# Kernel tuning notes

Measured on AMD Instinct MI355X. Metric: run time of the kernel, lower is better.

## Reference

```python
import jax, jax.numpy as jnp
import numpy as np

N, E, NFEAT, HID, HEADS, NCLASS = 100000, 1600000, 256, 64, 1, 32


def gat_conv(x, src, dst, W, a_src, a_dst, b, H, C, concat):
    n = x.shape[0]
    h = (x @ W).reshape(n, H, C)                      # [N,H,C]
    a_s = (h * a_src).sum(-1)                          # [N,H]
    a_d = (h * a_dst).sum(-1)                          # [N,H]
    e = jax.nn.leaky_relu(a_s[src] + a_d[dst], 0.2)    # [E,H]
    emax = jax.ops.segment_max(e, dst, num_segments=n)
    emax = jnp.where(jnp.isfinite(emax), emax, 0.0)
    ex = jnp.exp(e - emax[dst])
    denom = jax.ops.segment_sum(ex, dst, num_segments=n)
    alpha = ex / (denom[dst] + 1e-16)                  # segment softmax over in-edges of dst
    msg = h[src] * alpha[:, :, None]                   # [E,H,C]
    out = jax.ops.segment_sum(msg, dst, num_segments=n)
    out = out.reshape(n, H * C) if concat else out.mean(axis=1)
    return out + b


def setup_inputs() -> dict:
    key = jax.random.key(0)
    ks = jax.random.split(key, 14)
    x = jax.random.normal(ks[0], (N, NFEAT), dtype=jnp.float32)
    edge_index = jax.random.randint(ks[1], (2, E), 0, N, dtype=jnp.int64)
    s = 0.05
    return {
        'x': x, 'edge_index': edge_index,
        'W1': jax.random.normal(ks[2], (NFEAT, HEADS * HID), jnp.float32) * s,
        'as1': jax.random.normal(ks[3], (HEADS, HID), jnp.float32) * s,
        'ad1': jax.random.normal(ks[4], (HEADS, HID), jnp.float32) * s,
        'b1': jnp.zeros((HEADS * HID,), jnp.float32),
        'W2': jax.random.normal(ks[5], (HEADS * HID, HEADS * HID), jnp.float32) * s,
        'as2': jax.random.normal(ks[6], (HEADS, HID), jnp.float32) * s,
        'ad2': jax.random.normal(ks[7], (HEADS, HID), jnp.float32) * s,
        'b2': jnp.zeros((HEADS * HID,), jnp.float32),
        'W3': jax.random.normal(ks[8], (HEADS * HID, HEADS * NCLASS), jnp.float32) * s,
        'as3': jax.random.normal(ks[9], (HEADS, NCLASS), jnp.float32) * s,
        'ad3': jax.random.normal(ks[10], (HEADS, NCLASS), jnp.float32) * s,
        'b3': jnp.zeros((NCLASS,), jnp.float32),
    }


def reference(x, edge_index, W1, as1, ad1, b1, W2, as2, ad2, b2, W3, as3, ad3, b3):
    # add self loops (PyG GATConv add_self_loops=True)
    loop = jnp.arange(N, dtype=edge_index.dtype)
    src = jnp.concatenate([edge_index[0], loop])
    dst = jnp.concatenate([edge_index[1], loop])
    out = jax.nn.leaky_relu(gat_conv(x, src, dst, W1, as1, ad1, b1, HEADS, HID, True), 0.01)
    out = jax.nn.leaky_relu(gat_conv(out, src, dst, W2, as2, ad2, b2, HEADS, HID, True), 0.01)
    out = gat_conv(out, src, dst, W3, as3, ad3, b3, HEADS, NCLASS, False)
    return out
```

## Files before the change

kernel.cpp:

```cpp
#include <hip/hip_runtime.h>

#define NN 100000
#define NE 1600000
#define NF 256
#define HD 64
#define NC 32

#define BKS 8
#define NBK ((NN + 255) >> 8)
#define CHUNK 4096
#define NBLK ((NE + CHUNK - 1) / CHUNK)

__device__ __forceinline__ float lrelu02(float x) { return fmaxf(x, 0.2f * x); }


__global__ __launch_bounds__(256) void bucket_hist(const int* __restrict__ dst, int* __restrict__ gcnt) {
    __shared__ int hist[NBK];
    int tid = threadIdx.x;
    for (int i = tid; i < NBK; i += 256) hist[i] = 0;
    __syncthreads();
    int base = blockIdx.x * CHUNK;
    #pragma unroll
    for (int k = 0; k < CHUNK / 256; k++) {
        int i = base + k * 256 + tid;
        if (i < NE) atomicAdd(&hist[dst[i] >> BKS], 1);
    }
    __syncthreads();
    for (int i = tid; i < NBK; i += 256) if (hist[i]) atomicAdd(&gcnt[i], hist[i]);
}

__global__ void bucket_scan(const int* __restrict__ gcnt, int* __restrict__ gbase, int* __restrict__ gcur) {
    __shared__ int sh[512];
    int tid = threadIdx.x;
    int v = (tid < NBK) ? gcnt[tid] : 0;
    sh[tid] = v;
    __syncthreads();
    for (int d = 1; d < 512; d <<= 1) {
        int t = (tid >= d) ? sh[tid - d] : 0;
        __syncthreads();
        sh[tid] += t;
        __syncthreads();
    }
    if (tid < NBK) { int ex = sh[tid] - v; gbase[tid] = ex; gcur[tid] = ex; }
}

__global__ __launch_bounds__(256) void bin_edges(const int* __restrict__ src, const int* __restrict__ dst,
                                                 int* __restrict__ gcur, int2* __restrict__ ebuf) {
    __shared__ int hist[NBK];
    __shared__ int excl[NBK];
    __shared__ int runbase[NBK];
    __shared__ int ssum[256];
    __shared__ int2 sorted[CHUNK];
    int tid = threadIdx.x;
    int base = blockIdx.x * CHUNK;
    int n = NE - base; if (n > CHUNK) n = CHUNK;

    for (int i = tid; i < NBK; i += 256) hist[i] = 0;
    __syncthreads();

    int2 ed[CHUNK / 256];
    int bk[CHUNK / 256];
    #pragma unroll
    for (int k = 0; k < CHUNK / 256; k++) {
        int i = base + k * 256 + tid;
        if (i < NE) {
            ed[k] = make_int2(src[i], dst[i]);
            bk[k] = ed[k].y >> BKS;
            atomicAdd(&hist[bk[k]], 1);
        } else bk[k] = -1;
    }
    __syncthreads();
    int h0 = (2 * tid < NBK) ? hist[2 * tid] : 0;
    int h1 = (2 * tid + 1 < NBK) ? hist[2 * tid + 1] : 0;
    ssum[tid] = h0 + h1;
    __syncthreads();
    for (int d = 1; d < 256; d <<= 1) {
        int t = (tid >= d) ? ssum[tid - d] : 0;
        __syncthreads();
        ssum[tid] += t;
        __syncthreads();
    }
    int pref = ssum[tid] - (h0 + h1);
    if (2 * tid < NBK) excl[2 * tid] = pref;
    if (2 * tid + 1 < NBK) excl[2 * tid + 1] = pref + h0;
    for (int b = tid; b < NBK; b += 256) {
        int c = hist[b];
        runbase[b] = c ? atomicAdd(&gcur[b], c) : 0;
    }
    __syncthreads();
    #pragma unroll
    for (int k = 0; k < CHUNK / 256; k++) {
        if (bk[k] >= 0) {
            int r = atomicAdd(&excl[bk[k]], 1);
            sorted[r] = ed[k];
        }
    }
    __syncthreads();
    for (int i = tid; i < n; i += 256) {
        int2 e = sorted[i];
        int b = e.y >> BKS;
        int local_rank = i - (excl[b] - hist[b]);
        ebuf[runbase[b] + local_rank] = e;
    }
}

__global__ __launch_bounds__(256) void bucket_csr(const int2* __restrict__ ebuf, const int* __restrict__ gbase,
                                                  const int* __restrict__ gcnt,
                                                  int* __restrict__ offs, int* __restrict__ csr) {
    __shared__ int hist[256], cur[256], ssum[256];
    int b = blockIdx.x, tid = threadIdx.x;
    int ebeg = gbase[b], cnt = gcnt[b];
    int node0 = b << BKS;
    hist[tid] = 0;
    __syncthreads();
    for (int i = ebeg + tid; i < ebeg + cnt; i += 256)
        atomicAdd(&hist[ebuf[i].y & 255], 1);
    __syncthreads();
    int v = hist[tid];
    ssum[tid] = v;
    __syncthreads();
    for (int d = 1; d < 256; d <<= 1) {
        int t = (tid >= d) ? ssum[tid - d] : 0;
        __syncthreads();
        ssum[tid] += t;
        __syncthreads();
    }
    int ex = ebeg + ssum[tid] - v;
    cur[tid] = ex;
    int nnode = NN - node0; if (nnode > 256) nnode = 256;
    if (tid < nnode) offs[node0 + tid] = ex;
    if (b == NBK - 1 && tid == nnode - 1) offs[NN] = ebeg + cnt;
    __syncthreads();
    for (int i = ebeg + tid; i < ebeg + cnt; i += 256) {
        int2 e = ebuf[i];
        int pos = atomicAdd(&cur[e.y & 255], 1);
        csr[pos] = e.x;
    }
}


template <int CIN, int COUT, int NPT, int CPT>
__global__ __launch_bounds__(256) void rb_gemm3(const float* __restrict__ in, const float* __restrict__ W,
                                                const float* __restrict__ a_s, const float* __restrict__ a_d,
                                                float* __restrict__ h, float* __restrict__ asv,
                                                float* __restrict__ adv) {
    const int KC  = 32;
    const int CG  = COUT / CPT;
    const int NG  = 256 / CG;
    const int BN  = NG * NPT;
    const int BNP = BN + 4;
    const int NP4 = NPT / 4;
    const int CP4 = CPT / 4;
    __shared__ float xsT[KC * BNP];
    __shared__ float Wl[KC * COUT];

    int tid = threadIdx.x;
    int cg  = tid % CG;
    int ng  = tid / CG;
    int c0  = cg * CPT;
    int n0  = ng * NPT;
    int n0base = blockIdx.x * BN;

    float4 acc[NPT][CP4];
    #pragma unroll
    for (int i = 0; i < NPT; i++)
        #pragma unroll
        for (int j = 0; j < CP4; j++) acc[i][j] = make_float4(0.f, 0.f, 0.f, 0.f);

    for (int k0 = 0; k0 < CIN; k0 += KC) {
        __syncthreads();
        #pragma unroll
        for (int f = tid; f < BN * KC / 4; f += 256) {
            int n = f >> 3;
            int q = f & 7;
            int gn = n0base + n;
            float4 v = make_float4(0.f, 0.f, 0.f, 0.f);
            if (gn < NN) v = *(const float4*)&in[(size_t)gn * CIN + k0 + q * 4];
            xsT[(q * 4 + 0) * BNP + n] = v.x;
            xsT[(q * 4 + 1) * BNP + n] = v.y;
            xsT[(q * 4 + 2) * BNP + n] = v.z;
            xsT[(q * 4 + 3) * BNP + n] = v.w;
        }
        #pragma unroll
        for (int f = tid; f < KC * COUT / 4; f += 256)
            *(float4*)&Wl[f * 4] = *(const float4*)&W[(size_t)k0 * COUT + f * 4];
        __syncthreads();
        #pragma unroll 2
        for (int k = 0; k < KC; k++) {
            float4 xv[NP4];
            #pragma unroll
            for (int p = 0; p < NP4; p++) xv[p] = *(const float4*)&xsT[k * BNP + n0 + p * 4];
            float4 wv[CP4];
            #pragma unroll
            for (int j = 0; j < CP4; j++) wv[j] = *(const float4*)&Wl[k * COUT + c0 + j * 4];
            #pragma unroll
            for (int i = 0; i < NPT; i++) {
                float xc = (i & 3) == 0 ? xv[i >> 2].x : (i & 3) == 1 ? xv[i >> 2].y
                         : (i & 3) == 2 ? xv[i >> 2].z : xv[i >> 2].w;
                #pragma unroll
                for (int j = 0; j < CP4; j++) {
                    acc[i][j].x += xc * wv[j].x; acc[i][j].y += xc * wv[j].y;
                    acc[i][j].z += xc * wv[j].z; acc[i][j].w += xc * wv[j].w;
                }
            }
        }
    }

    float4 As[CP4], Ad[CP4];
    #pragma unroll
    for (int j = 0; j < CP4; j++) {
        As[j] = *(const float4*)&a_s[c0 + j * 4];
        Ad[j] = *(const float4*)&a_d[c0 + j * 4];
    }
    #pragma unroll
    for (int i = 0; i < NPT; i++) {
        int gn = n0base + n0 + i;
        if (gn < NN) {
            #pragma unroll
            for (int j = 0; j < CP4; j++)
                *(float4*)&h[(size_t)gn * COUT + c0 + j * 4] = acc[i][j];
        }
        float vs = 0.f, vd = 0.f;
        #pragma unroll
        for (int j = 0; j < CP4; j++) {
            vs += acc[i][j].x * As[j].x + acc[i][j].y * As[j].y
                + acc[i][j].z * As[j].z + acc[i][j].w * As[j].w;
            vd += acc[i][j].x * Ad[j].x + acc[i][j].y * Ad[j].y
                + acc[i][j].z * Ad[j].z + acc[i][j].w * Ad[j].w;
        }
        #pragma unroll
        for (int off = 1; off < CG; off <<= 1) { vs += __shfl_xor(vs, off); vd += __shfl_xor(vd, off); }
        if (cg == 0 && gn < NN) { asv[gn] = vs; adv[gn] = vd; }
    }
}


template <int C, bool ACT>
__global__ __launch_bounds__(256) void gat_agg(const float* __restrict__ h, const float* __restrict__ asv,
                                               const float* __restrict__ adv, const int* __restrict__ offs,
                                               const int* __restrict__ csr,
                                               const float* __restrict__ bias, float* __restrict__ out) {
    const int LPR = C / 4;
    const int G = 64 / LPR;
    const float4* h4 = (const float4*)h;
    int lane = threadIdx.x & 63;
    int v = blockIdx.x * 4 + (threadIdx.x >> 6);
    int beg = offs[v], end = offs[v + 1];
    int g = lane / LPR, r = lane % LPR;
    float adv_v = adv[v];

    float4 acc = {0.f, 0.f, 0.f, 0.f};
    float dsum = 0.f;
    #pragma unroll 4
    for (int e = beg + g; e < end; e += G) {
        int s = csr[e];
        float ww = __expf(lrelu02(asv[s] + adv_v));
        float4 hv = h4[(size_t)s * LPR + r];
        dsum += ww;
        acc.x += ww * hv.x; acc.y += ww * hv.y; acc.z += ww * hv.z; acc.w += ww * hv.w;
    }
    #pragma unroll
    for (int off = LPR; off < 64; off <<= 1) {
        acc.x += __shfl_xor(acc.x, off);
        acc.y += __shfl_xor(acc.y, off);
        acc.z += __shfl_xor(acc.z, off);
        acc.w += __shfl_xor(acc.w, off);
        dsum += __shfl_xor(dsum, off);
    }
    if (g == 0) {
        float selfw = __expf(lrelu02(asv[v] + adv_v));
        float4 hs = h4[(size_t)v * LPR + r];
        acc.x += selfw * hs.x; acc.y += selfw * hs.y;
        acc.z += selfw * hs.z; acc.w += selfw * hs.w;
        dsum += selfw;
        float inv = 1.f / (dsum + 1e-16f);
        float4 bb = ((const float4*)bias)[r];
        float4 o;
        o.x = acc.x * inv + bb.x; o.y = acc.y * inv + bb.y;
        o.z = acc.z * inv + bb.z; o.w = acc.w * inv + bb.w;
        if (ACT) {
            o.x = fmaxf(o.x, 0.01f * o.x); o.y = fmaxf(o.y, 0.01f * o.y);
            o.z = fmaxf(o.z, 0.01f * o.z); o.w = fmaxf(o.w, 0.01f * o.w);
        }
        ((float4*)out)[(size_t)v * LPR + r] = o;
    }
}


extern "C" void kernel_launch(void* const* d_in, const int* in_sizes, int n_in,
                              void* d_out, int out_size, void* d_ws, size_t ws_size,
                              hipStream_t stream) {
    const float* x   = (const float*)d_in[0];
    const int*   ei  = (const int*)d_in[1];
    const float* W1  = (const float*)d_in[2];
    const float* as1 = (const float*)d_in[3];
    const float* ad1 = (const float*)d_in[4];
    const float* b1  = (const float*)d_in[5];
    const float* W2  = (const float*)d_in[6];
    const float* as2 = (const float*)d_in[7];
    const float* ad2 = (const float*)d_in[8];
    const float* b2  = (const float*)d_in[9];
    const float* W3  = (const float*)d_in[10];
    const float* as3 = (const float*)d_in[11];
    const float* ad3 = (const float*)d_in[12];
    const float* b3  = (const float*)d_in[13];
    float* out = (float*)d_out;

    const int* srcp = ei;
    const int* dstp = ei + NE;

    char* w = (char*)d_ws;
    float* h     = (float*)w;   w += sizeof(float) * (size_t)NN * HD;
    float* featB = (float*)w;   w += sizeof(float) * (size_t)NN * HD;
    float* asv   = (float*)w;   w += sizeof(float) * NN;
    float* advv  = (float*)w;   w += sizeof(float) * NN;
    int* offs    = (int*)w;     w += sizeof(int) * (NN + 1);
    int* csr     = (int*)w;     w += sizeof(int) * (size_t)NE;
    int2* ebuf   = (int2*)w;    w += sizeof(int2) * (size_t)NE;
    int* gcnt    = (int*)w;     w += sizeof(int) * NBK;
    int* gbase   = (int*)w;     w += sizeof(int) * NBK;
    int* gcur    = (int*)w;     w += sizeof(int) * NBK;

    const int GB = (NN + 255) / 256;

    hipMemsetAsync(gcnt, 0, sizeof(int) * NBK, stream);
    bucket_hist<<<NBLK, 256, 0, stream>>>(dstp, gcnt);
    bucket_scan<<<1, 512, 0, stream>>>(gcnt, gbase, gcur);
    bin_edges<<<NBLK, 256, 0, stream>>>(srcp, dstp, gcur, ebuf);
    bucket_csr<<<NBK, 256, 0, stream>>>(ebuf, gbase, gcnt, offs, csr);

    rb_gemm3<NF, HD, 8, 8><<<GB, 256, 0, stream>>>(x, W1, as1, ad1, h, asv, advv);
    gat_agg<HD, true><<<NN / 4, 256, 0, stream>>>(h, asv, advv, offs, csr, b1, featB);

    rb_gemm3<HD, HD, 8, 8><<<GB, 256, 0, stream>>>(featB, W2, as2, ad2, h, asv, advv);
    gat_agg<HD, true><<<NN / 4, 256, 0, stream>>>(h, asv, advv, offs, csr, b2, featB);

    rb_gemm3<HD, NC, 4, 8><<<GB, 256, 0, stream>>>(featB, W3, as3, ad3, h, asv, advv);
    gat_agg<NC, false><<<NN / 4, 256, 0, stream>>>(h, asv, advv, offs, csr, b3, out);
}
```

Before: 500.4 us.

## Replace FP32 register-blocked GEMMs with split-bf16 MFMA GEMMs

Replaces the scalar FP32 register-tiled projection GEMM with a matrix-core kernel using bf16 MFMA 16x16x32. Accuracy is kept near FP32 by splitting each operand into high and low bf16 parts and issuing three MFMAs per tile. The attention-score dot products stay fused into the epilogue. The intent is to move the GEMM FLOPs onto matrix cores. In exchange, every tile load now pays for conversion and splitting, and the output stores become scalar, strided writes per lane.

Result: faster. 461.2 us (-7.8%).

```diff
diff --git a/kernel.cpp b/kernel.cpp
--- a/kernel.cpp
+++ b/kernel.cpp
@@ -12,6 +12,18 @@
 #define NBLK ((NE + CHUNK - 1) / CHUNK)
 
 __device__ __forceinline__ float lrelu02(float x) { return fmaxf(x, 0.2f * x); }
+
+typedef __attribute__((ext_vector_type(8))) short bf16x8;
+typedef __attribute__((ext_vector_type(4))) float f32x4;
+
+__device__ __forceinline__ unsigned short f2bf(float f) {
+    unsigned int u = __float_as_uint(f);
+    unsigned int r = u + 0x7FFFu + ((u >> 16) & 1u);
+    return (unsigned short)(r >> 16);
+}
+__device__ __forceinline__ float bf2f(unsigned short s) {
+    return __uint_as_float(((unsigned int)s) << 16);
+}
 
 
 __global__ __launch_bounds__(256) void bucket_hist(const int* __restrict__ dst, int* __restrict__ gcnt) {
@@ -139,98 +151,119 @@
 }
 
 
-template <int CIN, int COUT, int NPT, int CPT>
-__global__ __launch_bounds__(256) void rb_gemm3(const float* __restrict__ in, const float* __restrict__ W,
-                                                const float* __restrict__ a_s, const float* __restrict__ a_d,
-                                                float* __restrict__ h, float* __restrict__ asv,
-                                                float* __restrict__ adv) {
+template <int CIN, int COUT>
+__global__ __launch_bounds__(256) void mfma_gemm(const float* __restrict__ in, const float* __restrict__ W,
+                                                 const float* __restrict__ a_s, const float* __restrict__ a_d,
+                                                 float* __restrict__ h, float* __restrict__ asv,
+                                                 float* __restrict__ adv) {
     const int KC  = 32;
-    const int CG  = COUT / CPT;
-    const int NG  = 256 / CG;
-    const int BN  = NG * NPT;
-    const int BNP = BN + 4;
-    const int NP4 = NPT / 4;
-    const int CP4 = CPT / 4;
-    __shared__ float xsT[KC * BNP];
-    __shared__ float Wl[KC * COUT];
+    const int BM  = 128;
+    const int RS  = 40;
+    const int NCT = COUT / 16;
+    const int NCH = CIN / KC;
+    __shared__ unsigned short Ah[BM * RS];
+    __shared__ unsigned short Al[BM * RS];
+    __shared__ unsigned short Bh[COUT * RS];
+    __shared__ unsigned short Bl[COUT * RS];
 
     int tid = threadIdx.x;
-    int cg  = tid % CG;
-    int ng  = tid / CG;
-    int c0  = cg * CPT;
-    int n0  = ng * NPT;
-    int n0base = blockIdx.x * BN;
-
-    float4 acc[NPT][CP4];
-    #pragma unroll
-    for (int i = 0; i < NPT; i++)
-        #pragma unroll
-        for (int j = 0; j < CP4; j++) acc[i][j] = make_float4(0.f, 0.f, 0.f, 0.f);
-
-    for (int k0 = 0; k0 < CIN; k0 += KC) {
-        __syncthreads();
-        #pragma unroll
-        for (int f = tid; f < BN * KC / 4; f += 256) {
-            int n = f >> 3;
+    int lane = tid & 63;
+    int wave = tid >> 6;
+    int fr = lane & 15;
+    int kg = lane >> 4;
+    int n0base = blockIdx.x * BM;
+
+    f32x4 acc[2][NCT];
+    #pragma unroll
+    for (int rt = 0; rt < 2; rt++)
+        #pragma unroll
+        for (int ct = 0; ct < NCT; ct++) acc[rt][ct] = (f32x4){0.f, 0.f, 0.f, 0.f};
+
+    for (int t = 0; t < NCH; t++) {
+        int k0 = t * KC;
+        __syncthreads();
+        unsigned int* Ahu = (unsigned int*)Ah;
+        unsigned int* Alu = (unsigned int*)Al;
+        #pragma unroll
+        for (int f = tid; f < BM * KC / 4; f += 256) {
+            int row = f >> 3;
             int q = f & 7;
-            int gn = n0base + n;
+            int gn = n0base + row;
             float4 v = make_float4(0.f, 0.f, 0.f, 0.f);
             if (gn < NN) v = *(const float4*)&in[(size_t)gn * CIN + k0 + q * 4];
-            xsT[(q * 4 + 0) * BNP + n] = v.x;
-            xsT[(q * 4 + 1) * BNP + n] = v.y;
-            xsT[(q * 4 + 2) * BNP + n] = v.z;
-            xsT[(q * 4 + 3) * BNP + n] = v.w;
-        }
-        #pragma unroll
-        for (int f = tid; f < KC * COUT / 4; f += 256)
-            *(float4*)&Wl[f * 4] = *(const float4*)&W[(size_t)k0 * COUT + f * 4];
-        __syncthreads();
-        #pragma unroll 2
-        for (int k = 0; k < KC; k++) {
-            float4 xv[NP4];
+            unsigned short h0 = f2bf(v.x), h1 = f2bf(v.y), h2 = f2bf(v.z), h3 = f2bf(v.w);
+            unsigned short l0 = f2bf(v.x - bf2f(h0)), l1 = f2bf(v.y - bf2f(h1));
+            unsigned short l2 = f2bf(v.z - bf2f(h2)), l3 = f2bf(v.w - bf2f(h3));
+            int wi = row * (RS / 2) + q * 2;
+            Ahu[wi]     = (unsigned int)h0 | ((unsigned int)h1 << 16);
+            Ahu[wi + 1] = (unsigned int)h2 | ((unsigned int)h3 << 16);
+            Alu[wi]     = (unsigned int)l0 | ((unsigned int)l1 << 16);
+            Alu[wi + 1] = (unsigned int)l2 | ((unsigned int)l3 << 16);
+        }
+        #pragma unroll
+        for (int f = tid; f < KC * COUT / 4; f += 256) {
+            int k = f / (COUT / 4);
+            int c = (f % (COUT / 4)) * 4;
+            float4 v = *(const float4*)&W[(size_t)(k0 + k) * COUT + c];
+            unsigned short h0 = f2bf(v.x), h1 = f2bf(v.y), h2 = f2bf(v.z), h3 = f2bf(v.w);
+            Bh[(c + 0) * RS + k] = h0;  Bl[(c + 0) * RS + k] = f2bf(v.x - bf2f(h0));
+            Bh[(c + 1) * RS + k] = h1;  Bl[(c + 1) * RS + k] = f2bf(v.y - bf2f(h1));
+            Bh[(c + 2) * RS + k] = h2;  Bl[(c + 2) * RS + k] = f2bf(v.z - bf2f(h2));
+            Bh[(c + 3) * RS + k] = h3;  Bl[(c + 3) * RS + k] = f2bf(v.w - bf2f(h3));
+        }
+        __syncthreads();
+        bf16x8 ah[2], al[2], bh[NCT], bl[NCT];
+        #pragma unroll
+        for (int rt = 0; rt < 2; rt++) {
+            int row = wave * 32 + rt * 16 + fr;
+            ah[rt] = *(const bf16x8*)&Ah[row * RS + kg * 8];
+            al[rt] = *(const bf16x8*)&Al[row * RS + kg * 8];
+        }
+        #pragma unroll
+        for (int ct = 0; ct < NCT; ct++) {
+            int col = ct * 16 + fr;
+            bh[ct] = *(const bf16x8*)&Bh[col * RS + kg * 8];
+            bl[ct] = *(const bf16x8*)&Bl[col * RS + kg * 8];
+        }
+        #pragma unroll
+        for (int rt = 0; rt < 2; rt++)
             #pragma unroll
-            for (int p = 0; p < NP4; p++) xv[p] = *(const float4*)&xsT[k * BNP + n0 + p * 4];
-            float4 wv[CP4];
+            for (int ct = 0; ct < NCT; ct++) {
+                acc[rt][ct] = __builtin_amdgcn_mfma_f32_16x16x32_bf16(ah[rt], bh[ct], acc[rt][ct], 0, 0, 0);
+                acc[rt][ct] = __builtin_amdgcn_mfma_f32_16x16x32_bf16(ah[rt], bl[ct], acc[rt][ct], 0, 0, 0);
+                acc[rt][ct] = __builtin_amdgcn_mfma_f32_16x16x32_bf16(al[rt], bh[ct], acc[rt][ct], 0, 0, 0);
+            }
+    }
+
+    float As_l[NCT], Ad_l[NCT];
+    #pragma unroll
+    for (int ct = 0; ct < NCT; ct++) {
+        As_l[ct] = a_s[ct * 16 + fr];
+        Ad_l[ct] = a_d[ct * 16 + fr];
+    }
+    #pragma unroll
+    for (int rt = 0; rt < 2; rt++) {
+        #pragma unroll
+        for (int r = 0; r < 4; r++) {
+            int row = n0base + wave * 32 + rt * 16 + kg * 4 + r;
+            if (row < NN) {
+                #pragma unroll
+                for (int ct = 0; ct < NCT; ct++)
+                    h[(size_t)row * COUT + ct * 16 + fr] = acc[rt][ct][r];
+            }
+            float ps = 0.f, pd = 0.f;
             #pragma unroll
-            for (int j = 0; j < CP4; j++) wv[j] = *(const float4*)&Wl[k * COUT + c0 + j * 4];
+            for (int ct = 0; ct < NCT; ct++) {
+                ps += acc[rt][ct][r] * As_l[ct];
+                pd += acc[rt][ct][r] * Ad_l[ct];
+            }
             #pragma unroll
-            for (int i = 0; i < NPT; i++) {
-                float xc = (i & 3) == 0 ? xv[i >> 2].x : (i & 3) == 1 ? xv[i >> 2].y
-                         : (i & 3) == 2 ? xv[i >> 2].z : xv[i >> 2].w;
-                #pragma unroll
-                for (int j = 0; j < CP4; j++) {
-                    acc[i][j].x += xc * wv[j].x; acc[i][j].y += xc * wv[j].y;
-                    acc[i][j].z += xc * wv[j].z; acc[i][j].w += xc * wv[j].w;
-                }
+            for (int off = 1; off < 16; off <<= 1) {
+                ps += __shfl_xor(ps, off);
+                pd += __shfl_xor(pd, off);
             }
-        }
-    }
-
-    float4 As[CP4], Ad[CP4];
-    #pragma unroll
-    for (int j = 0; j < CP4; j++) {
-        As[j] = *(const float4*)&a_s[c0 + j * 4];
-        Ad[j] = *(const float4*)&a_d[c0 + j * 4];
-    }
-    #pragma unroll
-    for (int i = 0; i < NPT; i++) {
-        int gn = n0base + n0 + i;
-        if (gn < NN) {
-            #pragma unroll
-            for (int j = 0; j < CP4; j++)
-                *(float4*)&h[(size_t)gn * COUT + c0 + j * 4] = acc[i][j];
-        }
-        float vs = 0.f, vd = 0.f;
-        #pragma unroll
-        for (int j = 0; j < CP4; j++) {
-            vs += acc[i][j].x * As[j].x + acc[i][j].y * As[j].y
-                + acc[i][j].z * As[j].z + acc[i][j].w * As[j].w;
-            vd += acc[i][j].x * Ad[j].x + acc[i][j].y * Ad[j].y
-                + acc[i][j].z * Ad[j].z + acc[i][j].w * Ad[j].w;
-        }
-        #pragma unroll
-        for (int off = 1; off < CG; off <<= 1) { vs += __shfl_xor(vs, off); vd += __shfl_xor(vd, off); }
-        if (cg == 0 && gn < NN) { asv[gn] = vs; adv[gn] = vd; }
+            if (fr == 0 && row < NN) { asv[row] = ps; adv[row] = pd; }
+        }
     }
 }
 
@@ -321,7 +354,7 @@
     int* gbase   = (int*)w;     w += sizeof(int) * NBK;
     int* gcur    = (int*)w;     w += sizeof(int) * NBK;
 
-    const int GB = (NN + 255) / 256;
+    const int GBM = (NN + 127) / 128;
 
     hipMemsetAsync(gcnt, 0, sizeof(int) * NBK, stream);
     bucket_hist<<<NBLK, 256, 0, stream>>>(dstp, gcnt);
@@ -329,12 +362,12 @@
     bin_edges<<<NBLK, 256, 0, stream>>>(srcp, dstp, gcur, ebuf);
     bucket_csr<<<NBK, 256, 0, stream>>>(ebuf, gbase, gcnt, offs, csr);
 
-    rb_gemm3<NF, HD, 8, 8><<<GB, 256, 0, stream>>>(x, W1, as1, ad1, h, asv, advv);
+    mfma_gemm<NF, HD><<<GBM, 256, 0, stream>>>(x, W1, as1, ad1, h, asv, advv);
     gat_agg<HD, true><<<NN / 4, 256, 0, stream>>>(h, asv, advv, offs, csr, b1, featB);
 
-    rb_gemm3<HD, HD, 8, 8><<<GB, 256, 0, stream>>>(featB, W2, as2, ad2, h, asv, advv);
+    mfma_gemm<HD, HD><<<GBM, 256, 0, stream>>>(featB, W2, as2, ad2, h, asv, advv);
     gat_agg<HD, true><<<NN / 4, 256, 0, stream>>>(h, asv, advv, offs, csr, b2, featB);
 
-    rb_gemm3<HD, NC, 4, 8><<<GB, 256, 0, stream>>>(featB, W3, as3, ad3, h, asv, advv);
+    mfma_gemm<HD, NC><<<GBM, 256, 0, stream>>>(featB, W3, as3, ad3, h, asv, advv);
     gat_agg<NC, false><<<NN / 4, 256, 0, stream>>>(h, asv, advv, offs, csr, b3, out);
 }
```
